# Kernel tuning notes

Measured on AMD Instinct MI355X. Metric: run time of the kernel, lower is better.

## Reference

```python
import jax, jax.numpy as jnp
import numpy as np


def median_filter(image, kernel_size):
    """kxk sliding-window median with reflect padding, same spatial size.
    image: [B, C, H, W] float. kernel_size: odd Python int."""
    k = int(kernel_size)
    p = k // 2
    B, C, H, W = image.shape
    xp = jnp.pad(image, ((0, 0), (0, 0), (p, p), (p, p)), mode='reflect')
    # k*k shifted views stacked on a new last axis: [B, C, H, W, k*k]
    windows = jnp.stack(
        [xp[:, :, i:i + H, j:j + W] for i in range(k) for j in range(k)],
        axis=-1,
    )
    # k odd -> k*k odd -> exact middle element (matches torch.median selection)
    return jnp.median(windows, axis=-1)


def setup_inputs() -> dict:
    key = jax.random.key(0)
    k1, _ = jax.random.split(key)
    image = jax.random.uniform(k1, (8, 3, 512, 512), dtype=jnp.float32)
    mask = jnp.ones((8, 1, 512, 512), dtype=jnp.float32)
    return {"image": image, "mask": mask, "kernel_size": 5}


def reference(image, mask, kernel_size):
    med = median_filter(image, kernel_size)
    # passthrough=True: (median - image).detach() + image
    out = image + jax.lax.stop_gradient(med - image)
    return (out, mask)
```

## Files before the change

### kernel.cpp

```cpp
#include <hip/hip_runtime.h>
#include <cstddef>
#include <cstdint>


#define OTW 256
#define OTH 16

using u32 = uint32_t;

__device__ __forceinline__ u32 pmin(u32 a, u32 b) {
    u32 r;
    asm("v_pk_min_f16 %0, %1, %2" : "=v"(r) : "v"(a), "v"(b));
    return r;
}
__device__ __forceinline__ u32 pmax(u32 a, u32 b) {
    u32 r;
    asm("v_pk_max_f16 %0, %1, %2" : "=v"(r) : "v"(a), "v"(b));
    return r;
}
__device__ __forceinline__ void cep(u32& a, u32& b) {
    u32 lo = pmin(a, b);
    u32 hi = pmax(a, b);
    a = lo;
    b = hi;
}

typedef __fp16 h2_t __attribute__((ext_vector_type(2)));

__device__ __forceinline__ u32 pkrtz(float a, float b) {
    h2_t v = __builtin_amdgcn_cvt_pkrtz(a, b);
    u32 u;
    __builtin_memcpy(&u, &v, 4);
    return u;
}
__device__ __forceinline__ float lo16(u32 v) {
    unsigned short s = (unsigned short)(v & 0xffffu);
    __fp16 h;
    __builtin_memcpy(&h, &s, 2);
    return (float)h;
}
__device__ __forceinline__ float hi16(u32 v) {
    unsigned short s = (unsigned short)(v >> 16);
    __fp16 h;
    __builtin_memcpy(&h, &s, 2);
    return (float)h;
}

__device__ __forceinline__ void sort5p(u32 x[5]) {
    cep(x[0], x[1]); cep(x[3], x[4]); cep(x[2], x[4]); cep(x[2], x[3]);
    cep(x[0], x[3]); cep(x[0], x[2]); cep(x[1], x[4]); cep(x[1], x[3]);
    cep(x[1], x[2]);
}

__device__ __forceinline__ void oem22p(u32 x0, u32 x1, u32 y0, u32 y1,
                                       u32 z[4]) {
    u32 d0 = pmin(x0, y0), d1 = pmax(x0, y0);
    u32 e0 = pmin(x1, y1), e1 = pmax(x1, y1);
    z[0] = d0;
    z[1] = pmin(d1, e0);
    z[2] = pmax(d1, e0);
    z[3] = e1;
}

__device__ __forceinline__ void oem33p(u32 x0, u32 x1, u32 x2, u32 y0, u32 y1,
                                       u32 y2, u32 z[6]) {
    u32 d[4];
    oem22p(x0, x2, y0, y2, d);
    u32 e0 = pmin(x1, y1);
    u32 e1 = pmax(x1, y1);
    z[0] = d[0];
    z[1] = pmin(d[1], e0); z[2] = pmax(d[1], e0);
    z[3] = pmin(d[2], e1); z[4] = pmax(d[2], e1);
    z[5] = d[3];
}

__device__ __forceinline__ void oem55p(const u32 x[5], const u32 y[5],
                                       u32 z[10]) {
    u32 d[6];
    oem33p(x[0], x[2], x[4], y[0], y[2], y[4], d);
    u32 e[4];
    oem22p(x[1], x[3], y[1], y[3], e);
    z[0] = d[0];
    z[1] = pmin(d[1], e[0]); z[2] = pmax(d[1], e[0]);
    z[3] = pmin(d[2], e[1]); z[4] = pmax(d[2], e[1]);
    z[5] = pmin(d[3], e[2]); z[6] = pmax(d[3], e[2]);
    z[7] = pmin(d[4], e[3]); z[8] = pmax(d[4], e[3]);
    z[9] = d[5];
}

__device__ __forceinline__ void oem1010_mid_p(const u32 a[10], const u32 b[10],
                                              u32 u[6]) {
    u32 ae[5] = {a[0], a[2], a[4], a[6], a[8]};
    u32 be[5] = {b[0], b[2], b[4], b[6], b[8]};
    u32 ao[5] = {a[1], a[3], a[5], a[7], a[9]};
    u32 bo[5] = {b[1], b[3], b[5], b[7], b[9]};
    u32 d[10], e[10];
    oem55p(ae, be, d);
    oem55p(ao, bo, e);
    u[0] = pmin(d[4], e[3]); u[1] = pmax(d[4], e[3]);
    u[2] = pmin(d[5], e[4]); u[3] = pmax(d[5], e[4]);
    u[4] = pmin(d[6], e[5]); u[5] = pmax(d[6], e[5]);
}

__device__ __forceinline__ u32 oem65_z5_p(const u32 u[6], const u32 v[5]) {
    u32 d[6];
    oem33p(u[0], u[2], u[4], v[0], v[2], v[4], d);
    u32 dp1 = pmax(u[1], v[1]);
    u32 t1 = pmin(dp1, u[5]);
    u32 e2 = pmax(t1, pmin(u[3], v[3]));
    return pmin(d[3], e2);
}

__device__ __forceinline__ void medrow_p(const u32 c[8][5], u32 med4[4]) {
    u32 M12[10], M34[10], M56[10];
    oem55p(c[1], c[2], M12);
    oem55p(c[3], c[4], M34);
    u32 u[6];
    oem1010_mid_p(M12, M34, u);
    med4[0] = oem65_z5_p(u, c[0]);
    med4[1] = oem65_z5_p(u, c[5]);
    oem55p(c[5], c[6], M56);
    oem1010_mid_p(M34, M56, u);
    med4[2] = oem65_z5_p(u, c[2]);
    med4[3] = oem65_z5_p(u, c[7]);
}

__device__ __forceinline__ int reflect_idx(int i, int n) {
    i = i < 0 ? -i : i;
    i = i >= n ? 2 * n - 2 - i : i;
    return i;
}

#define MAXK 7
__device__ __noinline__ void generic_path(const float* __restrict__ src,
                                          float* __restrict__ dst, int k,
                                          int H, int W, int ox, int oy) {
    if (k < 1 || k > MAXK || (k & 1) == 0) return;
    if (k == 1) {
#pragma unroll
        for (int yy = 0; yy < 2; ++yy)
#pragma unroll
            for (int xx = 0; xx < 4; ++xx)
                dst[(size_t)(oy + yy) * W + ox + xx] =
                    src[(size_t)(oy + yy) * W + ox + xx];
        return;
    }
    const int p = k / 2;
    const int n = k * k;
    const int m = n / 2;
    float win[MAXK * MAXK];
    for (int yy = 0; yy < 2; ++yy) {
        for (int xx = 0; xx < 4; ++xx) {
            int x = ox + xx, y = oy + yy;
            int cnt = 0;
            for (int dy = -p; dy <= p; ++dy) {
                int gy = reflect_idx(y + dy, H);
                for (int dx = -p; dx <= p; ++dx) {
                    int gx = reflect_idx(x + dx, W);
                    win[cnt++] = src[(size_t)gy * W + gx];
                }
            }
            for (int a = 0; a <= m; ++a) {
                int mi = a;
                for (int b = a + 1; b < n; ++b)
                    if (win[b] < win[mi]) mi = b;
                float tv = win[a];
                win[a] = win[mi];
                win[mi] = tv;
            }
            dst[(size_t)y * W + x] = win[m];
        }
    }
}

__global__ __launch_bounds__(512) void median5_kernel(
    const float* __restrict__ img, const float* __restrict__ mask,
    float* __restrict__ out, const int* __restrict__ kptr, int H, int W,
    int nimg, long img_total) {
    const int tx = threadIdx.x;
    const int ty = threadIdx.y;
    const int x0 = blockIdx.x * OTW;
    const int y0 = blockIdx.y * OTH;
    const int z = blockIdx.z;

    if (z >= nimg) {
        const size_t base = (size_t)(z - nimg) * H * W;
        const int ox = x0 + 4 * tx;
        const int oy = y0 + 2 * ty;
        const float* ms = mask + base + (size_t)oy * W + ox;
        float* md = out + img_total + base + (size_t)oy * W + ox;
        *reinterpret_cast<float4*>(md) = *reinterpret_cast<const float4*>(ms);
        *reinterpret_cast<float4*>(md + W) =
            *reinterpret_cast<const float4*>(ms + W);
        return;
    }

    const float* __restrict__ src = img + (size_t)z * H * W;
    const int k = *kptr;
    if (k != 5) {
        generic_path(src, out + (size_t)z * H * W, k, H, W, x0 + 4 * tx,
                     y0 + 2 * ty);
        return;
    }

    __shared__ float tile[20][260];

    const int tid = ty * 64 + tx;

#pragma unroll
    for (int p = 0; p < 3; ++p) {
        int idx = tid + 512 * p;
        if (idx < 20 * 64) {
            int r = idx >> 6;
            int c4 = idx & 63;
            int gy = reflect_idx(y0 - 2 + r, H);
            float4 v = *reinterpret_cast<const float4*>(
                &src[(size_t)gy * W + x0 + 4 * c4]);
            *reinterpret_cast<float4*>(&tile[r][4 * c4]) = v;
        }
    }
    if (tid < 80) {
        int r = tid >> 2;
        int j = tid & 3;
        int gx = reflect_idx(x0 + ((j < 2) ? (j - 2) : (254 + j)), W);
        int gy = reflect_idx(y0 - 2 + r, H);
        tile[r][256 + j] = src[(size_t)gy * W + gx];
    }
    __syncthreads();

    const int cA = (tx == 0) ? 256 : 4 * tx - 2;
    const int cB = 4 * tx;
    const int cD = (tx == 63) ? 258 : 4 * tx + 4;

    u32 P[8][5];
    float prev[8];
    {
        const float* row = &tile[2 * ty][0];
        float2 v0 = *reinterpret_cast<const float2*>(row + cA);
        float4 v1 = *reinterpret_cast<const float4*>(row + cB);
        float2 v3 = *reinterpret_cast<const float2*>(row + cD);
        prev[0] = v0.x; prev[1] = v0.y;
        prev[2] = v1.x; prev[3] = v1.y;
        prev[4] = v1.z; prev[5] = v1.w;
        prev[6] = v3.x; prev[7] = v3.y;
    }
#pragma unroll
    for (int r = 1; r < 6; ++r) {
        const float* row = &tile[2 * ty + r][0];
        float2 v0 = *reinterpret_cast<const float2*>(row + cA);
        float4 v1 = *reinterpret_cast<const float4*>(row + cB);
        float2 v3 = *reinterpret_cast<const float2*>(row + cD);
        float cur[8];
        cur[0] = v0.x; cur[1] = v0.y;
        cur[2] = v1.x; cur[3] = v1.y;
        cur[4] = v1.z; cur[5] = v1.w;
        cur[6] = v3.x; cur[7] = v3.y;
#pragma unroll
        for (int j = 0; j < 8; ++j) {
            P[j][r - 1] = pkrtz(prev[j], cur[j]);
            prev[j] = cur[j];
        }
    }
#pragma unroll
    for (int j = 0; j < 8; ++j) sort5p(P[j]);

    u32 medp[4];
    medrow_p(P, medp);

    const int ox = x0 + 4 * tx;
    const int oyA = y0 + 2 * ty;
    float* dst = out + (size_t)z * H * W + (size_t)oyA * W + ox;
    *reinterpret_cast<float4*>(dst) =
        make_float4(lo16(medp[0]), lo16(medp[1]), lo16(medp[2]), lo16(medp[3]));
    *reinterpret_cast<float4*>(dst + W) =
        make_float4(hi16(medp[0]), hi16(medp[1]), hi16(medp[2]), hi16(medp[3]));
}

extern "C" void kernel_launch(void* const* d_in, const int* in_sizes, int n_in,
                              void* d_out, int out_size, void* d_ws,
                              size_t ws_size, hipStream_t stream) {
    const float* img = (const float*)d_in[0];
    const float* mask = (const float*)d_in[1];
    const int* kptr = (const int*)d_in[2];
    float* out = (float*)d_out;

    const int H = 512, W = 512;
    const long img_elems = in_sizes[0];
    const long mask_elems = in_sizes[1];
    const int nimg = (int)(img_elems / ((long)H * W));
    const int nmask = (int)(mask_elems / ((long)H * W));

    dim3 block(64, 8);
    dim3 grid(W / OTW, H / OTH, nimg + nmask);
    median5_kernel<<<grid, block, 0, stream>>>(img, mask, out, kptr, H, W,
                                               nimg, img_elems);
}
```

Baseline: 24.85 us.

## Double output rows per thread to cut halo overhead in median tile

Doubles the tile height so each thread computes four output rows instead of two. It loads 8 smem rows per thread and builds two overlapping packed-column sets, reusing the shared middle rows. This lowers the halo load overhead per output and halves the number of blocks. In exchange, register pressure is higher, the grid is smaller and the LDS tile is larger, which may reduce occupancy.

New measurement: 25.29 us. About the same (+1.8%).

```diff
diff --git a/kernel.cpp b/kernel.cpp
--- a/kernel.cpp
+++ b/kernel.cpp
@@ -4,7 +4,7 @@
 
 
 #define OTW 256
-#define OTH 16
+#define OTH 32
 
 using u32 = uint32_t;
 
@@ -138,7 +138,7 @@
     if (k < 1 || k > MAXK || (k & 1) == 0) return;
     if (k == 1) {
 #pragma unroll
-        for (int yy = 0; yy < 2; ++yy)
+        for (int yy = 0; yy < 4; ++yy)
 #pragma unroll
             for (int xx = 0; xx < 4; ++xx)
                 dst[(size_t)(oy + yy) * W + ox + xx] =
@@ -149,7 +149,7 @@
     const int n = k * k;
     const int m = n / 2;
     float win[MAXK * MAXK];
-    for (int yy = 0; yy < 2; ++yy) {
+    for (int yy = 0; yy < 4; ++yy) {
         for (int xx = 0; xx < 4; ++xx) {
             int x = ox + xx, y = oy + yy;
             int cnt = 0;
@@ -186,12 +186,13 @@
     if (z >= nimg) {
         const size_t base = (size_t)(z - nimg) * H * W;
         const int ox = x0 + 4 * tx;
-        const int oy = y0 + 2 * ty;
+        const int oy = y0 + 4 * ty;
         const float* ms = mask + base + (size_t)oy * W + ox;
         float* md = out + img_total + base + (size_t)oy * W + ox;
-        *reinterpret_cast<float4*>(md) = *reinterpret_cast<const float4*>(ms);
-        *reinterpret_cast<float4*>(md + W) =
-            *reinterpret_cast<const float4*>(ms + W);
+#pragma unroll
+        for (int yy = 0; yy < 4; ++yy)
+            *reinterpret_cast<float4*>(md + (size_t)yy * W) =
+                *reinterpret_cast<const float4*>(ms + (size_t)yy * W);
         return;
     }
 
@@ -199,18 +200,18 @@
     const int k = *kptr;
     if (k != 5) {
         generic_path(src, out + (size_t)z * H * W, k, H, W, x0 + 4 * tx,
-                     y0 + 2 * ty);
+                     y0 + 4 * ty);
         return;
     }
 
-    __shared__ float tile[20][260];
+    __shared__ float tile[36][260];
 
     const int tid = ty * 64 + tx;
 
 #pragma unroll
-    for (int p = 0; p < 3; ++p) {
+    for (int p = 0; p < 5; ++p) {
         int idx = tid + 512 * p;
-        if (idx < 20 * 64) {
+        if (idx < 36 * 64) {
             int r = idx >> 6;
             int c4 = idx & 63;
             int gy = reflect_idx(y0 - 2 + r, H);
@@ -219,7 +220,7 @@
             *reinterpret_cast<float4*>(&tile[r][4 * c4]) = v;
         }
     }
-    if (tid < 80) {
+    if (tid < 144) {
         int r = tid >> 2;
         int j = tid & 3;
         int gx = reflect_idx(x0 + ((j < 2) ? (j - 2) : (254 + j)), W);
@@ -232,10 +233,10 @@
     const int cB = 4 * tx;
     const int cD = (tx == 63) ? 258 : 4 * tx + 4;
 
-    u32 P[8][5];
+    u32 P1[8][5], P2[8][5];
     float prev[8];
     {
-        const float* row = &tile[2 * ty][0];
+        const float* row = &tile[4 * ty][0];
         float2 v0 = *reinterpret_cast<const float2*>(row + cA);
         float4 v1 = *reinterpret_cast<const float4*>(row + cB);
         float2 v3 = *reinterpret_cast<const float2*>(row + cD);
@@ -245,8 +246,8 @@
         prev[6] = v3.x; prev[7] = v3.y;
     }
 #pragma unroll
-    for (int r = 1; r < 6; ++r) {
-        const float* row = &tile[2 * ty + r][0];
+    for (int r = 1; r < 8; ++r) {
+        const float* row = &tile[4 * ty + r][0];
         float2 v0 = *reinterpret_cast<const float2*>(row + cA);
         float4 v1 = *reinterpret_cast<const float4*>(row + cB);
         float2 v3 = *reinterpret_cast<const float2*>(row + cD);
@@ -257,23 +258,37 @@
         cur[6] = v3.x; cur[7] = v3.y;
 #pragma unroll
         for (int j = 0; j < 8; ++j) {
-            P[j][r - 1] = pkrtz(prev[j], cur[j]);
+            u32 pk = pkrtz(prev[j], cur[j]);
+            if (r - 1 <= 4) P1[j][r - 1] = pk;
+            if (r - 3 >= 0) P2[j][r - 3] = pk;
             prev[j] = cur[j];
         }
     }
-#pragma unroll
-    for (int j = 0; j < 8; ++j) sort5p(P[j]);
-
-    u32 medp[4];
-    medrow_p(P, medp);
 
     const int ox = x0 + 4 * tx;
-    const int oyA = y0 + 2 * ty;
+    const int oyA = y0 + 4 * ty;
     float* dst = out + (size_t)z * H * W + (size_t)oyA * W + ox;
-    *reinterpret_cast<float4*>(dst) =
-        make_float4(lo16(medp[0]), lo16(medp[1]), lo16(medp[2]), lo16(medp[3]));
-    *reinterpret_cast<float4*>(dst + W) =
-        make_float4(hi16(medp[0]), hi16(medp[1]), hi16(medp[2]), hi16(medp[3]));
+
+#pragma unroll
+    for (int j = 0; j < 8; ++j) sort5p(P1[j]);
+    {
+        u32 medp[4];
+        medrow_p(P1, medp);
+        *reinterpret_cast<float4*>(dst) = make_float4(
+            lo16(medp[0]), lo16(medp[1]), lo16(medp[2]), lo16(medp[3]));
+        *reinterpret_cast<float4*>(dst + W) = make_float4(
+            hi16(medp[0]), hi16(medp[1]), hi16(medp[2]), hi16(medp[3]));
+    }
+#pragma unroll
+    for (int j = 0; j < 8; ++j) sort5p(P2[j]);
+    {
+        u32 medp[4];
+        medrow_p(P2, medp);
+        *reinterpret_cast<float4*>(dst + 2 * (size_t)W) = make_float4(
+            lo16(medp[0]), lo16(medp[1]), lo16(medp[2]), lo16(medp[3]));
+        *reinterpret_cast<float4*>(dst + 3 * (size_t)W) = make_float4(
+            hi16(medp[0]), hi16(medp[1]), hi16(medp[2]), hi16(medp[3]));
+    }
 }
 
 extern "C" void kernel_launch(void* const* d_in, const int* in_sizes, int n_in,
```

## Halve per-thread output width to 2x2 and narrow tile to 128 columns

Applied to the files above, without the earlier changes.

Each thread now computes a 2x2 output patch instead of 4x2, with a 128-wide block tile, which doubles the block count and threads. This shortens per-thread register pressure and adds occupancy hint via launch_bounds(512,8). The cost is less reuse of sorted columns across outputs (6 columns sorted for 2 outputs instead of 8 for 4) and more halo loads per output, so total ALU work per pixel rises.

After: 24.93 us. About the same (+0.3%).

```diff
diff --git a/kernel.cpp b/kernel.cpp
--- a/kernel.cpp
+++ b/kernel.cpp
@@ -3,7 +3,7 @@
 #include <cstdint>
 
 
-#define OTW 256
+#define OTW 128
 #define OTH 16
 
 using u32 = uint32_t;
@@ -111,20 +111,6 @@
     return pmin(d[3], e2);
 }
 
-__device__ __forceinline__ void medrow_p(const u32 c[8][5], u32 med4[4]) {
-    u32 M12[10], M34[10], M56[10];
-    oem55p(c[1], c[2], M12);
-    oem55p(c[3], c[4], M34);
-    u32 u[6];
-    oem1010_mid_p(M12, M34, u);
-    med4[0] = oem65_z5_p(u, c[0]);
-    med4[1] = oem65_z5_p(u, c[5]);
-    oem55p(c[5], c[6], M56);
-    oem1010_mid_p(M34, M56, u);
-    med4[2] = oem65_z5_p(u, c[2]);
-    med4[3] = oem65_z5_p(u, c[7]);
-}
-
 __device__ __forceinline__ int reflect_idx(int i, int n) {
     i = i < 0 ? -i : i;
     i = i >= n ? 2 * n - 2 - i : i;
@@ -140,7 +126,7 @@
 #pragma unroll
         for (int yy = 0; yy < 2; ++yy)
 #pragma unroll
-            for (int xx = 0; xx < 4; ++xx)
+            for (int xx = 0; xx < 2; ++xx)
                 dst[(size_t)(oy + yy) * W + ox + xx] =
                     src[(size_t)(oy + yy) * W + ox + xx];
         return;
@@ -150,7 +136,7 @@
     const int m = n / 2;
     float win[MAXK * MAXK];
     for (int yy = 0; yy < 2; ++yy) {
-        for (int xx = 0; xx < 4; ++xx) {
+        for (int xx = 0; xx < 2; ++xx) {
             int x = ox + xx, y = oy + yy;
             int cnt = 0;
             for (int dy = -p; dy <= p; ++dy) {
@@ -173,7 +159,7 @@
     }
 }
 
-__global__ __launch_bounds__(512) void median5_kernel(
+__global__ __launch_bounds__(512, 8) void median5_kernel(
     const float* __restrict__ img, const float* __restrict__ mask,
     float* __restrict__ out, const int* __restrict__ kptr, int H, int W,
     int nimg, long img_total) {
@@ -185,34 +171,34 @@
 
     if (z >= nimg) {
         const size_t base = (size_t)(z - nimg) * H * W;
-        const int ox = x0 + 4 * tx;
+        const int ox = x0 + 2 * tx;
         const int oy = y0 + 2 * ty;
         const float* ms = mask + base + (size_t)oy * W + ox;
         float* md = out + img_total + base + (size_t)oy * W + ox;
-        *reinterpret_cast<float4*>(md) = *reinterpret_cast<const float4*>(ms);
-        *reinterpret_cast<float4*>(md + W) =
-            *reinterpret_cast<const float4*>(ms + W);
+        *reinterpret_cast<float2*>(md) = *reinterpret_cast<const float2*>(ms);
+        *reinterpret_cast<float2*>(md + W) =
+            *reinterpret_cast<const float2*>(ms + W);
         return;
     }
 
     const float* __restrict__ src = img + (size_t)z * H * W;
     const int k = *kptr;
     if (k != 5) {
-        generic_path(src, out + (size_t)z * H * W, k, H, W, x0 + 4 * tx,
+        generic_path(src, out + (size_t)z * H * W, k, H, W, x0 + 2 * tx,
                      y0 + 2 * ty);
         return;
     }
 
-    __shared__ float tile[20][260];
+    __shared__ float tile[20][132];
 
     const int tid = ty * 64 + tx;
 
 #pragma unroll
-    for (int p = 0; p < 3; ++p) {
+    for (int p = 0; p < 2; ++p) {
         int idx = tid + 512 * p;
-        if (idx < 20 * 64) {
-            int r = idx >> 6;
-            int c4 = idx & 63;
+        if (idx < 20 * 32) {
+            int r = idx >> 5;
+            int c4 = idx & 31;
             int gy = reflect_idx(y0 - 2 + r, H);
             float4 v = *reinterpret_cast<const float4*>(
                 &src[(size_t)gy * W + x0 + 4 * c4]);
@@ -222,58 +208,59 @@
     if (tid < 80) {
         int r = tid >> 2;
         int j = tid & 3;
-        int gx = reflect_idx(x0 + ((j < 2) ? (j - 2) : (254 + j)), W);
+        int gx = reflect_idx(x0 + ((j < 2) ? (j - 2) : (126 + j)), W);
         int gy = reflect_idx(y0 - 2 + r, H);
-        tile[r][256 + j] = src[(size_t)gy * W + gx];
+        tile[r][128 + j] = src[(size_t)gy * W + gx];
     }
     __syncthreads();
 
-    const int cA = (tx == 0) ? 256 : 4 * tx - 2;
-    const int cB = 4 * tx;
-    const int cD = (tx == 63) ? 258 : 4 * tx + 4;
-
-    u32 P[8][5];
-    float prev[8];
+    const int cA = (tx == 0) ? 128 : 2 * tx - 2;
+    const int cB = 2 * tx;
+    const int cC = (tx == 63) ? 130 : 2 * tx + 2;
+
+    u32 P[6][5];
+    float prev[6];
     {
         const float* row = &tile[2 * ty][0];
         float2 v0 = *reinterpret_cast<const float2*>(row + cA);
-        float4 v1 = *reinterpret_cast<const float4*>(row + cB);
-        float2 v3 = *reinterpret_cast<const float2*>(row + cD);
+        float2 v1 = *reinterpret_cast<const float2*>(row + cB);
+        float2 v2 = *reinterpret_cast<const float2*>(row + cC);
         prev[0] = v0.x; prev[1] = v0.y;
         prev[2] = v1.x; prev[3] = v1.y;
-        prev[4] = v1.z; prev[5] = v1.w;
-        prev[6] = v3.x; prev[7] = v3.y;
+        prev[4] = v2.x; prev[5] = v2.y;
     }
 #pragma unroll
     for (int r = 1; r < 6; ++r) {
         const float* row = &tile[2 * ty + r][0];
         float2 v0 = *reinterpret_cast<const float2*>(row + cA);
-        float4 v1 = *reinterpret_cast<const float4*>(row + cB);
-        float2 v3 = *reinterpret_cast<const float2*>(row + cD);
-        float cur[8];
+        float2 v1 = *reinterpret_cast<const float2*>(row + cB);
+        float2 v2 = *reinterpret_cast<const float2*>(row + cC);
+        float cur[6];
         cur[0] = v0.x; cur[1] = v0.y;
         cur[2] = v1.x; cur[3] = v1.y;
-        cur[4] = v1.z; cur[5] = v1.w;
-        cur[6] = v3.x; cur[7] = v3.y;
-#pragma unroll
-        for (int j = 0; j < 8; ++j) {
+        cur[4] = v2.x; cur[5] = v2.y;
+#pragma unroll
+        for (int j = 0; j < 6; ++j) {
             P[j][r - 1] = pkrtz(prev[j], cur[j]);
             prev[j] = cur[j];
         }
     }
 #pragma unroll
-    for (int j = 0; j < 8; ++j) sort5p(P[j]);
-
-    u32 medp[4];
-    medrow_p(P, medp);
-
-    const int ox = x0 + 4 * tx;
-    const int oyA = y0 + 2 * ty;
-    float* dst = out + (size_t)z * H * W + (size_t)oyA * W + ox;
-    *reinterpret_cast<float4*>(dst) =
-        make_float4(lo16(medp[0]), lo16(medp[1]), lo16(medp[2]), lo16(medp[3]));
-    *reinterpret_cast<float4*>(dst + W) =
-        make_float4(hi16(medp[0]), hi16(medp[1]), hi16(medp[2]), hi16(medp[3]));
+    for (int j = 0; j < 6; ++j) sort5p(P[j]);
+
+    u32 M12[10], M34[10];
+    oem55p(P[1], P[2], M12);
+    oem55p(P[3], P[4], M34);
+    u32 u[6];
+    oem1010_mid_p(M12, M34, u);
+    u32 m0 = oem65_z5_p(u, P[0]);
+    u32 m1 = oem65_z5_p(u, P[5]);
+
+    const int ox = x0 + 2 * tx;
+    const int oy = y0 + 2 * ty;
+    float* dst = out + (size_t)z * H * W + (size_t)oy * W + ox;
+    *reinterpret_cast<float2*>(dst) = make_float2(lo16(m0), lo16(m1));
+    *reinterpret_cast<float2*>(dst + W) = make_float2(hi16(m0), hi16(m1));
 }
 
 extern "C" void kernel_launch(void* const* d_in, const int* in_sizes, int n_in,
```
